# Kernel optimization log

Hardware: AMD Instinct MI355X
Metric: run time of the kernel (lower is better)

The kernel has to match this reference:

```python
import jax, jax.numpy as jnp
import numpy as np

XYZ_MIN = -1.0
XYZ_MAX = 1.0
ALPHA_INIT = 0.01
ACT_SHIFT = float(np.log(1.0 / (1.0 - ALPHA_INIT) - 1.0))  # density bias shift
INTERVAL = 0.5  # stepsize * voxel_size_ratio
VIEWBASE_PE = 4


def trilinear(grid, pts):
    """grid: [C,X,Y,Z]; pts: [...,3] in world coords; align_corners=True trilinear."""
    gs = grid.shape[1:]
    size_f = jnp.asarray(gs, pts.dtype)
    u = (pts - XYZ_MIN) / (XYZ_MAX - XYZ_MIN) * (size_f - 1.0)
    u = jnp.clip(u, 0.0, size_f - 1.0)
    i0 = jnp.floor(u).astype(jnp.int32)
    i0 = jnp.minimum(i0, jnp.asarray(gs, jnp.int32) - 2)
    f = u - i0.astype(pts.dtype)
    x0, y0, z0 = i0[..., 0], i0[..., 1], i0[..., 2]
    x1, y1, z1 = x0 + 1, y0 + 1, z0 + 1
    fx, fy, fz = f[..., 0, None], f[..., 1, None], f[..., 2, None]
    g = lambda ix, iy, iz: jnp.moveaxis(grid[:, ix, iy, iz], 0, -1)  # [...,C]
    c00 = g(x0, y0, z0) * (1 - fz) + g(x0, y0, z1) * fz
    c01 = g(x0, y1, z0) * (1 - fz) + g(x0, y1, z1) * fz
    c10 = g(x1, y0, z0) * (1 - fz) + g(x1, y0, z1) * fz
    c11 = g(x1, y1, z0) * (1 - fz) + g(x1, y1, z1) * fz
    c0 = c00 * (1 - fy) + c01 * fy
    c1 = c10 * (1 - fy) + c11 * fy
    return c0 * (1 - fx) + c1 * fx


def setup_inputs() -> dict:
    key = jax.random.key(0)
    ks = jax.random.split(key, 8)
    N, S, G, C, W = 4096, 256, 160, 12, 128
    dim0 = 3 + 3 * VIEWBASE_PE * 2 + C  # 39
    pts = jax.random.uniform(ks[0], (N, S, 3), jnp.float32, minval=-1.0, maxval=1.0)
    viewdirs = jax.random.normal(ks[1], (N, 3), jnp.float32)
    density_grid = jax.random.normal(ks[2], (1, G, G, G), jnp.float32)
    k0_grid = jax.random.normal(ks[3], (C, G, G, G), jnp.float32)
    w0 = jax.random.normal(ks[4], (dim0, W), jnp.float32) * 0.1
    w1 = jax.random.normal(ks[5], (W, W), jnp.float32) * 0.1
    w2 = jax.random.normal(ks[6], (W, 3), jnp.float32) * 0.1
    return dict(pts=pts, viewdirs=viewdirs, density_grid=density_grid, k0_grid=k0_grid,
                w0=w0, b0=jnp.zeros((W,), jnp.float32), w1=w1, b1=jnp.zeros((W,), jnp.float32),
                w2=w2, b2=jnp.zeros((3,), jnp.float32))


def reference(pts, viewdirs, density_grid, k0_grid, w0, b0, w1, b1, w2, b2):
    # --- density query + Raw2Alpha: alpha = 1 - (1+exp(d+shift))^(-interval) ---
    dens = trilinear(density_grid, pts)[..., 0]  # [N,S]
    alpha = 1.0 - jnp.exp(-jax.nn.softplus(dens + ACT_SHIFT) * INTERVAL)
    # --- Alphas2Weights: per-ray exclusive transmittance cumprod ---
    T = jnp.cumprod(1.0 - alpha, axis=1)  # [N,S]
    T_excl = jnp.concatenate([jnp.ones_like(T[:, :1]), T[:, :-1]], axis=1)
    weights = alpha * T_excl  # [N,S]
    alphainv_last = T[:, -1]  # [N]
    # --- color feature grid + view positional encoding ---
    k0 = trilinear(k0_grid, pts)  # [N,S,C]
    vd = viewdirs / jnp.linalg.norm(viewdirs, axis=-1, keepdims=True)  # [N,3]
    freqs = (2.0 ** jnp.arange(VIEWBASE_PE)).astype(vd.dtype)
    vf = (vd[..., None] * freqs).reshape(vd.shape[0], -1)  # [N,12]
    emb = jnp.concatenate([vd, jnp.sin(vf), jnp.cos(vf)], axis=-1)  # [N,27]
    feat = jnp.concatenate(
        [k0, jnp.broadcast_to(emb[:, None, :], k0.shape[:2] + (emb.shape[-1],))], axis=-1)  # [N,S,39]
    # --- rgbnet MLP (depth 3) ---
    h = jax.nn.relu(feat @ w0 + b0)
    h = jax.nn.relu(h @ w1 + b1)
    rgb = jax.nn.sigmoid(h @ w2 + b2)  # [N,S,3]
    # --- composite with white background ---
    rgb_marched = jnp.einsum('ns,nsc->nc', weights, rgb) + alphainv_last[:, None]
    return rgb_marched
```

## Files before the change

### kernel.cpp

```cpp
#include <hip/hip_runtime.h>

#define G      160
#define G3     (G*G*G)
#define NRAYS  4096
#define SAMP   256
#define CK0    12
#define HID    128

#define ACT_SHIFT (-4.59511985013459f)

#define FS 72
#define HS 136

typedef __attribute__((ext_vector_type(8))) short bf16x8;
typedef __attribute__((ext_vector_type(4))) float f32x4;

__device__ __forceinline__ unsigned short f2bf(float x) {
    unsigned u = __float_as_uint(x);
    unsigned r = u + 0x7fffu + ((u >> 16) & 1u);
    return (unsigned short)(r >> 16);
}
__device__ __forceinline__ float bflo(unsigned u) { return __uint_as_float(u << 16); }
__device__ __forceinline__ float bfhi(unsigned u) { return __uint_as_float(u & 0xffff0000u); }
__device__ __forceinline__ unsigned pack2(float a, float b) {
    return (unsigned)f2bf(a) | ((unsigned)f2bf(b) << 16);
}

__global__ __launch_bounds__(256) void prepass_kernel(
        const float* __restrict__ dgrid,
        const float* __restrict__ kgrid,
        unsigned short* __restrict__ vox)
{
    int v4 = (blockIdx.x * 256 + threadIdx.x) * 4;
    if (v4 >= G3) return;
    union F4 { float4 v; float f[4]; };
    F4 d; d.v = *reinterpret_cast<const float4*>(dgrid + v4);
    F4 kk[CK0];
#pragma unroll
    for (int c = 0; c < CK0; c++)
        kk[c].v = *reinterpret_cast<const float4*>(kgrid + (size_t)c * G3 + v4);
#pragma unroll
    for (int i = 0; i < 4; i++) {
        uint4 qa, qb;
        qa.x = pack2(d.f[i],      kk[0].f[i]);
        qa.y = pack2(kk[1].f[i],  kk[2].f[i]);
        qa.z = pack2(kk[3].f[i],  kk[4].f[i]);
        qa.w = pack2(kk[5].f[i],  kk[6].f[i]);
        qb.x = pack2(kk[7].f[i],  kk[8].f[i]);
        qb.y = pack2(kk[9].f[i],  kk[10].f[i]);
        qb.z = pack2(kk[11].f[i], 0.0f);
        qb.w = 0u;
        uint4* dst = reinterpret_cast<uint4*>(vox + (size_t)(v4 + i) * 16);
        dst[0] = qa;
        dst[1] = qb;
    }
}

__global__ void pack_weights(const float* __restrict__ w0,
                             const float* __restrict__ w1,
                             const float* __restrict__ w2,
                             unsigned short* __restrict__ w0p,
                             unsigned short* __restrict__ w1p,
                             unsigned short* __restrict__ w2p)
{
    int t = threadIdx.x;
    for (int idx = t; idx < 16 * 512; idx += 256) {
        int f = idx >> 9, r = idx & 511, l = r >> 3, j = r & 7;
        int nt = f >> 1, ks = f & 1;
        int k = ks * 32 + ((l >> 4) << 3) + j;
        int n = nt * 16 + (l & 15);
        w0p[idx] = (k < 39) ? f2bf(w0[k * HID + n]) : (unsigned short)0;
    }
    for (int idx = t; idx < 32 * 512; idx += 256) {
        int f = idx >> 9, r = idx & 511, l = r >> 3, j = r & 7;
        int nt = f >> 2, ks = f & 3;
        int k = ks * 32 + ((l >> 4) << 3) + j;
        int n = nt * 16 + (l & 15);
        w1p[idx] = f2bf(w1[k * HID + n]);
    }
    for (int idx = t; idx < 4 * 512; idx += 256) {
        int f = idx >> 9, r = idx & 511, l = r >> 3, j = r & 7;
        int ks = f;
        int k = ks * 32 + ((l >> 4) << 3) + j;
        int n = (l & 15);
        w2p[idx] = (n < 3) ? f2bf(w2[k * 3 + n]) : (unsigned short)0;
    }
}

__global__ __launch_bounds__(256) void dvgo_mfma(
        const float* __restrict__ pts,
        const float* __restrict__ viewdirs,
        const unsigned short* __restrict__ vox,
        const unsigned short* __restrict__ w0p,
        const unsigned short* __restrict__ w1p,
        const unsigned short* __restrict__ w2p,
        const float* __restrict__ b0, const float* __restrict__ b1,
        const float* __restrict__ b2,
        float* __restrict__ out)
{
    __shared__ unsigned short s_mem[SAMP * HS];
    __shared__ float s_alpha[SAMP];
    __shared__ float s_P[SAMP];
    __shared__ float s_out[4];

    const int n = blockIdx.x;
    const int t = threadIdx.x;
    const int lane = t & 63;
    const int wv = t >> 6;
    const int wbase = wv << 6;
    const int c    = lane & 15;
    const int quad = lane >> 4;

    if (t < 4) s_out[t] = 0.0f;

    const float* p = pts + ((size_t)n * SAMP + t) * 3;
    float pc[3] = {p[0], p[1], p[2]};
    int   i0[3];
    float fr[3];
#pragma unroll
    for (int d = 0; d < 3; d++) {
        float uu = (pc[d] + 1.0f) * 0.5f * (float)(G - 1);
        uu = fminf(fmaxf(uu, 0.0f), (float)(G - 1));
        int i = (int)floorf(uu);
        if (i > G - 2) i = G - 2;
        i0[d] = i;
        fr[d] = uu - (float)i;
    }

    float dens = 0.0f;
    float k0v[CK0];
#pragma unroll
    for (int ch = 0; ch < CK0; ch++) k0v[ch] = 0.0f;

#pragma unroll
    for (int cx = 0; cx < 2; cx++) {
        float wx = cx ? fr[0] : 1.0f - fr[0];
#pragma unroll
        for (int cy = 0; cy < 2; cy++) {
            float wxy = wx * (cy ? fr[1] : 1.0f - fr[1]);
#pragma unroll
            for (int cz = 0; cz < 2; cz++) {
                float wgt = wxy * (cz ? fr[2] : 1.0f - fr[2]);
                int vidx = ((i0[0] + cx) * G + (i0[1] + cy)) * G + (i0[2] + cz);
                const uint4* q = reinterpret_cast<const uint4*>(vox) + (size_t)vidx * 2;
                uint4 A = q[0];
                uint4 B = q[1];
                dens    += wgt * bflo(A.x);
                k0v[0]  += wgt * bfhi(A.x);
                k0v[1]  += wgt * bflo(A.y);
                k0v[2]  += wgt * bfhi(A.y);
                k0v[3]  += wgt * bflo(A.z);
                k0v[4]  += wgt * bfhi(A.z);
                k0v[5]  += wgt * bflo(A.w);
                k0v[6]  += wgt * bfhi(A.w);
                k0v[7]  += wgt * bflo(B.x);
                k0v[8]  += wgt * bfhi(B.x);
                k0v[9]  += wgt * bflo(B.y);
                k0v[10] += wgt * bfhi(B.y);
                k0v[11] += wgt * bflo(B.z);
            }
        }
    }

    float xs = dens + ACT_SHIFT;
    float sp = (xs > 20.0f) ? xs : log1pf(expf(xs));
    float alpha = 1.0f - expf(-sp * 0.5f);
    s_alpha[t] = alpha;
    s_P[t] = 1.0f - alpha;

    float v0 = viewdirs[n * 3 + 0];
    float v1 = viewdirs[n * 3 + 1];
    float v2 = viewdirs[n * 3 + 2];
    float inv = 1.0f / sqrtf(v0 * v0 + v1 * v1 + v2 * v2);
    v0 *= inv; v1 *= inv; v2 *= inv;

    float feat[40];
#pragma unroll
    for (int ch = 0; ch < CK0; ch++) feat[ch] = k0v[ch];
    feat[12] = v0; feat[13] = v1; feat[14] = v2;
    {
        float vd3[3] = {v0, v1, v2};
#pragma unroll
        for (int i = 0; i < 3; i++) {
#pragma unroll
            for (int j = 0; j < 4; j++) {
                float a = vd3[i] * (float)(1 << j);
                feat[15 + i * 4 + j] = sinf(a);
                feat[27 + i * 4 + j] = cosf(a);
            }
        }
    }
    feat[39] = 0.0f;

#pragma unroll
    for (int ch = 0; ch < 8; ch++) {
        uint4 q;
        if (ch < 5) {
            q.x = pack2(feat[ch * 8 + 0], feat[ch * 8 + 1]);
            q.y = pack2(feat[ch * 8 + 2], feat[ch * 8 + 3]);
            q.z = pack2(feat[ch * 8 + 4], feat[ch * 8 + 5]);
            q.w = pack2(feat[ch * 8 + 6], feat[ch * 8 + 7]);
        } else {
            q.x = 0u; q.y = 0u; q.z = 0u; q.w = 0u;
        }
        *reinterpret_cast<uint4*>(&s_mem[t * FS + ch * 8]) = q;
    }

    __syncthreads();
#pragma unroll
    for (int off = 1; off < SAMP; off <<= 1) {
        float v = (t >= off) ? s_P[t - off] : 1.0f;
        __syncthreads();
        s_P[t] *= v;
        __syncthreads();
    }

    const f32x4 zf = {0.0f, 0.0f, 0.0f, 0.0f};

    bf16x8 a1[4][2];
#pragma unroll
    for (int mt = 0; mt < 4; mt++)
#pragma unroll
        for (int ks = 0; ks < 2; ks++)
            a1[mt][ks] = *reinterpret_cast<const bf16x8*>(
                &s_mem[(wbase + mt * 16 + c) * FS + ks * 32 + quad * 8]);
    __syncthreads();

    const uint4* w0q = reinterpret_cast<const uint4*>(w0p);
#pragma unroll
    for (int nt = 0; nt < 8; nt++) {
        union { uint4 q; bf16x8 s; } bA, bB;
        bA.q = w0q[(nt * 2 + 0) * 64 + lane];
        bB.q = w0q[(nt * 2 + 1) * 64 + lane];
        f32x4 acc[4];
#pragma unroll
        for (int mt = 0; mt < 4; mt++) {
            f32x4 tmp = __builtin_amdgcn_mfma_f32_16x16x32_bf16(a1[mt][0], bA.s, zf, 0, 0, 0);
            acc[mt]   = __builtin_amdgcn_mfma_f32_16x16x32_bf16(a1[mt][1], bB.s, tmp, 0, 0, 0);
        }
        float bias = b0[nt * 16 + c];
#pragma unroll
        for (int mt = 0; mt < 4; mt++)
#pragma unroll
            for (int r = 0; r < 4; r++) {
                float h = fmaxf(acc[mt][r] + bias, 0.0f);
                s_mem[(wbase + mt * 16 + quad * 4 + r) * HS + nt * 16 + c] = f2bf(h);
            }
    }

    bf16x8 a2[4][4];
#pragma unroll
    for (int mt = 0; mt < 4; mt++)
#pragma unroll
        for (int ks = 0; ks < 4; ks++)
            a2[mt][ks] = *reinterpret_cast<const bf16x8*>(
                &s_mem[(wbase + mt * 16 + c) * HS + ks * 32 + quad * 8]);

    const uint4* w1q = reinterpret_cast<const uint4*>(w1p);
#pragma unroll
    for (int nt = 0; nt < 8; nt++) {
        f32x4 acc[4] = {zf, zf, zf, zf};
#pragma unroll
        for (int ks = 0; ks < 4; ks++) {
            union { uint4 q; bf16x8 s; } bb;
            bb.q = w1q[(nt * 4 + ks) * 64 + lane];
#pragma unroll
            for (int mt = 0; mt < 4; mt++)
                acc[mt] = __builtin_amdgcn_mfma_f32_16x16x32_bf16(a2[mt][ks], bb.s, acc[mt], 0, 0, 0);
        }
        float bias = b1[nt * 16 + c];
#pragma unroll
        for (int mt = 0; mt < 4; mt++)
#pragma unroll
            for (int r = 0; r < 4; r++) {
                float h = fmaxf(acc[mt][r] + bias, 0.0f);
                s_mem[(wbase + mt * 16 + quad * 4 + r) * HS + nt * 16 + c] = f2bf(h);
            }
    }

    bf16x8 a3[4][4];
#pragma unroll
    for (int mt = 0; mt < 4; mt++)
#pragma unroll
        for (int ks = 0; ks < 4; ks++)
            a3[mt][ks] = *reinterpret_cast<const bf16x8*>(
                &s_mem[(wbase + mt * 16 + c) * HS + ks * 32 + quad * 8]);

    const uint4* w2q = reinterpret_cast<const uint4*>(w2p);
    f32x4 acc3[4] = {zf, zf, zf, zf};
#pragma unroll
    for (int ks = 0; ks < 4; ks++) {
        union { uint4 q; bf16x8 s; } bb;
        bb.q = w2q[ks * 64 + lane];
#pragma unroll
        for (int mt = 0; mt < 4; mt++)
            acc3[mt] = __builtin_amdgcn_mfma_f32_16x16x32_bf16(a3[mt][ks], bb.s, acc3[mt], 0, 0, 0);
    }

    float b2c = (c < 3) ? b2[c] : 0.0f;
    float csum = 0.0f;
#pragma unroll
    for (int mt = 0; mt < 4; mt++)
#pragma unroll
        for (int r = 0; r < 4; r++) {
            int m = wbase + mt * 16 + quad * 4 + r;
            float pre = acc3[mt][r] + b2c;
            float sg = 1.0f / (1.0f + expf(-pre));
            float Texcl = (m == 0) ? 1.0f : s_P[m - 1];
            float wgt = s_alpha[m] * Texcl;
            csum += wgt * sg;
        }
    csum += __shfl_xor(csum, 16);
    csum += __shfl_xor(csum, 32);
    if (quad == 0 && c < 3) atomicAdd(&s_out[c], csum);
    __syncthreads();
    if (t < 3) out[n * 3 + t] = s_out[t] + s_P[SAMP - 1];
}

__global__ __launch_bounds__(256, 2) void dvgo_fallback(
        const float* __restrict__ pts, const float* __restrict__ viewdirs,
        const float* __restrict__ dgrid, const float* __restrict__ kgrid,
        const float* __restrict__ w0, const float* __restrict__ b0,
        const float* __restrict__ w1, const float* __restrict__ b1,
        const float* __restrict__ w2, const float* __restrict__ b2,
        float* __restrict__ out)
{
    const int n = blockIdx.x;
    const int t = threadIdx.x;
    __shared__ float  s_alpha[SAMP];
    __shared__ float  s_P[SAMP];
    __shared__ float  s_h1[SAMP * 33];
    __shared__ float  s_red[12];

    const float* p = pts + ((size_t)n * SAMP + t) * 3;
    float pc[3] = {p[0], p[1], p[2]};
    int i0[3]; float fr[3];
#pragma unroll
    for (int d = 0; d < 3; d++) {
        float uu = (pc[d] + 1.0f) * 0.5f * (float)(G - 1);
        uu = fminf(fmaxf(uu, 0.0f), (float)(G - 1));
        int i = (int)floorf(uu);
        if (i > G - 2) i = G - 2;
        i0[d] = i; fr[d] = uu - (float)i;
    }
    float dens = 0.0f, k0v[CK0];
#pragma unroll
    for (int ch = 0; ch < CK0; ch++) k0v[ch] = 0.0f;
#pragma unroll
    for (int cx = 0; cx < 2; cx++)
#pragma unroll
        for (int cy = 0; cy < 2; cy++)
#pragma unroll
            for (int cz = 0; cz < 2; cz++) {
                float w = (cx ? fr[0] : 1.0f - fr[0]) * (cy ? fr[1] : 1.0f - fr[1]) * (cz ? fr[2] : 1.0f - fr[2]);
                int vidx = ((i0[0] + cx) * G + (i0[1] + cy)) * G + (i0[2] + cz);
                dens += w * dgrid[vidx];
#pragma unroll
                for (int ch = 0; ch < CK0; ch++) k0v[ch] += w * kgrid[(size_t)ch * G3 + vidx];
            }
    float xs = dens + ACT_SHIFT;
    float sp = (xs > 20.0f) ? xs : log1pf(expf(xs));
    float alpha = 1.0f - expf(-sp * 0.5f);
    s_alpha[t] = alpha; s_P[t] = 1.0f - alpha;
    __syncthreads();
#pragma unroll
    for (int off = 1; off < SAMP; off <<= 1) {
        float v = (t >= off) ? s_P[t - off] : 1.0f;
        __syncthreads();
        s_P[t] *= v;
        __syncthreads();
    }
    float v0 = viewdirs[n * 3 + 0], v1 = viewdirs[n * 3 + 1], v2 = viewdirs[n * 3 + 2];
    float inv = 1.0f / sqrtf(v0 * v0 + v1 * v1 + v2 * v2);
    v0 *= inv; v1 *= inv; v2 *= inv;
    float feat[39];
#pragma unroll
    for (int ch = 0; ch < CK0; ch++) feat[ch] = k0v[ch];
    feat[12] = v0; feat[13] = v1; feat[14] = v2;
    float vd3[3] = {v0, v1, v2};
#pragma unroll
    for (int i = 0; i < 3; i++)
#pragma unroll
        for (int j = 0; j < 4; j++) {
            float a = vd3[i] * (float)(1 << j);
            feat[15 + i * 4 + j] = sinf(a);
            feat[27 + i * 4 + j] = cosf(a);
        }
    float h1[HID];
#pragma unroll 1
    for (int ch = 0; ch < 4; ch++) {
        float acc[32];
#pragma unroll
        for (int j = 0; j < 32; j++) acc[j] = b0[ch * 32 + j];
#pragma unroll
        for (int k = 0; k < 39; k++) {
            float f = feat[k];
#pragma unroll
            for (int j = 0; j < 32; j++) acc[j] = fmaf(f, w0[k * HID + ch * 32 + j], acc[j]);
        }
#pragma unroll
        for (int j = 0; j < 32; j++) h1[ch * 32 + j] = fmaxf(acc[j], 0.0f);
    }
    float rgbpre[3] = {b2[0], b2[1], b2[2]};
#pragma unroll 1
    for (int ch = 0; ch < 4; ch++) {
        float acc[32];
#pragma unroll
        for (int j = 0; j < 32; j++) acc[j] = b1[ch * 32 + j];
#pragma unroll 4
        for (int k = 0; k < HID; k++) {
            float hk = h1[k];
#pragma unroll
            for (int j = 0; j < 32; j++) acc[j] = fmaf(hk, w1[k * HID + ch * 32 + j], acc[j]);
        }
#pragma unroll
        for (int j = 0; j < 32; j++) {
            float h2 = fmaxf(acc[j], 0.0f);
            int jj = ch * 32 + j;
            rgbpre[0] = fmaf(h2, w2[jj * 3 + 0], rgbpre[0]);
            rgbpre[1] = fmaf(h2, w2[jj * 3 + 1], rgbpre[1]);
            rgbpre[2] = fmaf(h2, w2[jj * 3 + 2], rgbpre[2]);
        }
    }
    float T_excl = (t == 0) ? 1.0f : s_P[t - 1];
    float wgt = s_alpha[t] * T_excl;
    float c0 = wgt / (1.0f + expf(-rgbpre[0]));
    float c1 = wgt / (1.0f + expf(-rgbpre[1]));
    float c2 = wgt / (1.0f + expf(-rgbpre[2]));
#pragma unroll
    for (int off = 32; off > 0; off >>= 1) {
        c0 += __shfl_down(c0, off);
        c1 += __shfl_down(c1, off);
        c2 += __shfl_down(c2, off);
    }
    if ((t & 63) == 0) {
        int wv = t >> 6;
        s_red[wv * 3 + 0] = c0; s_red[wv * 3 + 1] = c1; s_red[wv * 3 + 2] = c2;
    }
    __syncthreads();
    if (t == 0) {
        float alast = s_P[SAMP - 1];
        float o0 = alast, o1 = alast, o2 = alast;
#pragma unroll
        for (int wv = 0; wv < 4; wv++) {
            o0 += s_red[wv * 3 + 0]; o1 += s_red[wv * 3 + 1]; o2 += s_red[wv * 3 + 2];
        }
        out[n * 3 + 0] = o0; out[n * 3 + 1] = o1; out[n * 3 + 2] = o2;
    }
    (void)s_h1;
}

extern "C" void kernel_launch(void* const* d_in, const int* in_sizes, int n_in,
                              void* d_out, int out_size, void* d_ws, size_t ws_size,
                              hipStream_t stream) {
    const float* pts      = (const float*)d_in[0];
    const float* viewdirs = (const float*)d_in[1];
    const float* dgrid    = (const float*)d_in[2];
    const float* kgrid    = (const float*)d_in[3];
    const float* w0       = (const float*)d_in[4];
    const float* b0       = (const float*)d_in[5];
    const float* w1       = (const float*)d_in[6];
    const float* b1       = (const float*)d_in[7];
    const float* w2       = (const float*)d_in[8];
    const float* b2       = (const float*)d_in[9];
    float* out = (float*)d_out;

    const size_t VOXB = (size_t)G3 * 32;
    const size_t W0PE = 16 * 512, W1PE = 32 * 512, W2PE = 4 * 512;
    const size_t TOTB = VOXB + (W0PE + W1PE + W2PE) * 2;

    if (ws_size >= TOTB) {
        unsigned short* vox  = (unsigned short*)d_ws;
        unsigned short* w0pp = (unsigned short*)((char*)d_ws + VOXB);
        unsigned short* w1pp = w0pp + W0PE;
        unsigned short* w2pp = w1pp + W1PE;
        prepass_kernel<<<G3 / 4 / 256, 256, 0, stream>>>(dgrid, kgrid, vox);
        pack_weights<<<1, 256, 0, stream>>>(w0, w1, w2, w0pp, w1pp, w2pp);
        dvgo_mfma<<<NRAYS, 256, 0, stream>>>(pts, viewdirs, vox, w0pp, w1pp, w2pp,
                                             b0, b1, b2, out);
    } else {
        dvgo_fallback<<<NRAYS, SAMP, 0, stream>>>(pts, viewdirs, dgrid, kgrid,
                                                  w0, b0, w1, b1, w2, b2, out);
    }
}
```

Baseline: 551.5 us.

## Switch to fp16 MFMA, wave-scan transmittance, per-wave LDS slabs, parallel weight packing

Replaces bf16 storage and MFMA with fp16 (pkrtz conversion, half2 FMA trilinear accumulation) and moves density into the last half of each voxel record. The shared-memory cumprod with many block barriers becomes a wave shuffle scan plus a cross-wave prefix, and precomputed weights are stored once. The view-direction embedding is computed by a few threads and broadcast, per-wave LDS slabs remove block-wide syncs, and weight packing now runs over many blocks. Fast intrinsics (__expf, __logf, __sinf) replace precise ones, and fp16 accumulation of features adds precision and range risk.

Result: faster. 519.7 us (-5.8%).

```diff
diff --git a/kernel.cpp b/kernel.cpp
--- a/kernel.cpp
+++ b/kernel.cpp
@@ -1,4 +1,5 @@
 #include <hip/hip_runtime.h>
+#include <hip/hip_fp16.h>
 
 #define G      160
 #define G3     (G*G*G)
@@ -11,19 +12,16 @@
 
 #define FS 72
 #define HS 136
-
-typedef __attribute__((ext_vector_type(8))) short bf16x8;
-typedef __attribute__((ext_vector_type(4))) float f32x4;
-
-__device__ __forceinline__ unsigned short f2bf(float x) {
-    unsigned u = __float_as_uint(x);
-    unsigned r = u + 0x7fffu + ((u >> 16) & 1u);
-    return (unsigned short)(r >> 16);
-}
-__device__ __forceinline__ float bflo(unsigned u) { return __uint_as_float(u << 16); }
-__device__ __forceinline__ float bfhi(unsigned u) { return __uint_as_float(u & 0xffff0000u); }
-__device__ __forceinline__ unsigned pack2(float a, float b) {
-    return (unsigned)f2bf(a) | ((unsigned)f2bf(b) << 16);
+#define SLABH (64 * HS)
+
+typedef __attribute__((ext_vector_type(8))) _Float16 f16x8;
+typedef __attribute__((ext_vector_type(4))) float    f32x4;
+
+__device__ __forceinline__ unsigned pkrtz_u(float a, float b) {
+    typedef __attribute__((ext_vector_type(2))) __fp16 fp16v2;
+    union { fp16v2 h; unsigned u; } cv;
+    cv.h = __builtin_amdgcn_cvt_pkrtz(a, b);
+    return cv.u;
 }
 
 __global__ __launch_bounds__(256) void prepass_kernel(
@@ -42,48 +40,51 @@
 #pragma unroll
     for (int i = 0; i < 4; i++) {
         uint4 qa, qb;
-        qa.x = pack2(d.f[i],      kk[0].f[i]);
-        qa.y = pack2(kk[1].f[i],  kk[2].f[i]);
-        qa.z = pack2(kk[3].f[i],  kk[4].f[i]);
-        qa.w = pack2(kk[5].f[i],  kk[6].f[i]);
-        qb.x = pack2(kk[7].f[i],  kk[8].f[i]);
-        qb.y = pack2(kk[9].f[i],  kk[10].f[i]);
-        qb.z = pack2(kk[11].f[i], 0.0f);
-        qb.w = 0u;
+        qa.x = pkrtz_u(kk[0].f[i],  kk[1].f[i]);
+        qa.y = pkrtz_u(kk[2].f[i],  kk[3].f[i]);
+        qa.z = pkrtz_u(kk[4].f[i],  kk[5].f[i]);
+        qa.w = pkrtz_u(kk[6].f[i],  kk[7].f[i]);
+        qb.x = pkrtz_u(kk[8].f[i],  kk[9].f[i]);
+        qb.y = pkrtz_u(kk[10].f[i], kk[11].f[i]);
+        qb.z = 0u;
+        qb.w = pkrtz_u(0.0f, d.f[i]);
         uint4* dst = reinterpret_cast<uint4*>(vox + (size_t)(v4 + i) * 16);
         dst[0] = qa;
         dst[1] = qb;
     }
 }
 
-__global__ void pack_weights(const float* __restrict__ w0,
-                             const float* __restrict__ w1,
-                             const float* __restrict__ w2,
-                             unsigned short* __restrict__ w0p,
-                             unsigned short* __restrict__ w1p,
-                             unsigned short* __restrict__ w2p)
+#define W0PE (16 * 512)
+#define W1PE (32 * 512)
+#define W2PE (4 * 512)
+__global__ __launch_bounds__(256) void pack_weights(
+        const float* __restrict__ w0, const float* __restrict__ w1,
+        const float* __restrict__ w2,
+        unsigned short* __restrict__ w0p, unsigned short* __restrict__ w1p,
+        unsigned short* __restrict__ w2p)
 {
-    int t = threadIdx.x;
-    for (int idx = t; idx < 16 * 512; idx += 256) {
+    int idx = blockIdx.x * 256 + threadIdx.x;
+    if (idx < W0PE) {
         int f = idx >> 9, r = idx & 511, l = r >> 3, j = r & 7;
         int nt = f >> 1, ks = f & 1;
         int k = ks * 32 + ((l >> 4) << 3) + j;
-        int n = nt * 16 + (l & 15);
-        w0p[idx] = (k < 39) ? f2bf(w0[k * HID + n]) : (unsigned short)0;
-    }
-    for (int idx = t; idx < 32 * 512; idx += 256) {
-        int f = idx >> 9, r = idx & 511, l = r >> 3, j = r & 7;
+        int nn = nt * 16 + (l & 15);
+        w0p[idx] = (k < 39) ? __half_as_ushort(__float2half(w0[k * HID + nn]))
+                            : (unsigned short)0;
+    } else if (idx < W0PE + W1PE) {
+        int m = idx - W0PE;
+        int f = m >> 9, r = m & 511, l = r >> 3, j = r & 7;
         int nt = f >> 2, ks = f & 3;
         int k = ks * 32 + ((l >> 4) << 3) + j;
-        int n = nt * 16 + (l & 15);
-        w1p[idx] = f2bf(w1[k * HID + n]);
-    }
-    for (int idx = t; idx < 4 * 512; idx += 256) {
-        int f = idx >> 9, r = idx & 511, l = r >> 3, j = r & 7;
-        int ks = f;
+        int nn = nt * 16 + (l & 15);
+        w1p[m] = __half_as_ushort(__float2half(w1[k * HID + nn]));
+    } else if (idx < W0PE + W1PE + W2PE) {
+        int m = idx - W0PE - W1PE;
+        int ks = m >> 9, r = m & 511, l = r >> 3, j = r & 7;
         int k = ks * 32 + ((l >> 4) << 3) + j;
-        int n = (l & 15);
-        w2p[idx] = (n < 3) ? f2bf(w2[k * 3 + n]) : (unsigned short)0;
+        int nn = l & 15;
+        w2p[m] = (nn < 3) ? __half_as_ushort(__float2half(w2[k * 3 + nn]))
+                          : (unsigned short)0;
     }
 }
 
@@ -98,20 +99,43 @@
         const float* __restrict__ b2,
         float* __restrict__ out)
 {
-    __shared__ unsigned short s_mem[SAMP * HS];
-    __shared__ float s_alpha[SAMP];
-    __shared__ float s_P[SAMP];
-    __shared__ float s_out[4];
-
-    const int n = blockIdx.x;
-    const int t = threadIdx.x;
+    __shared__ __half s_mem[4 * SLABH];
+    __shared__ float  s_wgt[SAMP];
+    __shared__ float  s_wave[4];
+    __shared__ unsigned s_u[16];
+    __shared__ float  s_out[4];
+
+    const int n    = blockIdx.x;
+    const int t    = threadIdx.x;
     const int lane = t & 63;
-    const int wv = t >> 6;
+    const int wv   = t >> 6;
     const int wbase = wv << 6;
     const int c    = lane & 15;
     const int quad = lane >> 4;
+    __half* slab = s_mem + wv * SLABH;
+    const int lr = lane;
 
     if (t < 4) s_out[t] = 0.0f;
+
+    if (t < 14) {
+        float v0 = viewdirs[n * 3 + 0];
+        float v1 = viewdirs[n * 3 + 1];
+        float v2 = viewdirs[n * 3 + 2];
+        float inv = rsqrtf(v0 * v0 + v1 * v1 + v2 * v2);
+        float vd[3] = {v0 * inv, v1 * inv, v2 * inv};
+        float fv[2];
+#pragma unroll
+        for (int e = 0; e < 2; e++) {
+            int col = 12 + 2 * t + e;
+            float f;
+            if (col < 15)      f = vd[col - 12];
+            else if (col < 27) { int s = col - 15; f = __sinf(vd[s >> 2] * (float)(1 << (s & 3))); }
+            else if (col < 39) { int s = col - 27; f = __cosf(vd[s >> 2] * (float)(1 << (s & 3))); }
+            else               f = 0.0f;
+            fv[e] = f;
+        }
+        s_u[t + 2] = pkrtz_u(fv[0], fv[1]);
+    }
 
     const float* p = pts + ((size_t)n * SAMP + t) * 3;
     float pc[3] = {p[0], p[1], p[2]};
@@ -127,10 +151,9 @@
         fr[d] = uu - (float)i;
     }
 
+    __half2 accA0 = __float2half2_rn(0.0f), accA1 = accA0, accA2 = accA0, accA3 = accA0;
+    __half2 accB0 = accA0, accB1 = accA0;
     float dens = 0.0f;
-    float k0v[CK0];
-#pragma unroll
-    for (int ch = 0; ch < CK0; ch++) k0v[ch] = 0.0f;
 
 #pragma unroll
     for (int cx = 0; cx < 2; cx++) {
@@ -140,121 +163,105 @@
             float wxy = wx * (cy ? fr[1] : 1.0f - fr[1]);
 #pragma unroll
             for (int cz = 0; cz < 2; cz++) {
-                float wgt = wxy * (cz ? fr[2] : 1.0f - fr[2]);
+                float w = wxy * (cz ? fr[2] : 1.0f - fr[2]);
                 int vidx = ((i0[0] + cx) * G + (i0[1] + cy)) * G + (i0[2] + cz);
                 const uint4* q = reinterpret_cast<const uint4*>(vox) + (size_t)vidx * 2;
-                uint4 A = q[0];
-                uint4 B = q[1];
-                dens    += wgt * bflo(A.x);
-                k0v[0]  += wgt * bfhi(A.x);
-                k0v[1]  += wgt * bflo(A.y);
-                k0v[2]  += wgt * bfhi(A.y);
-                k0v[3]  += wgt * bflo(A.z);
-                k0v[4]  += wgt * bfhi(A.z);
-                k0v[5]  += wgt * bflo(A.w);
-                k0v[6]  += wgt * bfhi(A.w);
-                k0v[7]  += wgt * bflo(B.x);
-                k0v[8]  += wgt * bfhi(B.x);
-                k0v[9]  += wgt * bflo(B.y);
-                k0v[10] += wgt * bfhi(B.y);
-                k0v[11] += wgt * bflo(B.z);
+                union { uint4 q; __half2 h2[4]; } A, B;
+                A.q = q[0];
+                B.q = q[1];
+                __half2 wh = __half2half2(__float2half(w));
+                accA0 = __hfma2(wh, A.h2[0], accA0);
+                accA1 = __hfma2(wh, A.h2[1], accA1);
+                accA2 = __hfma2(wh, A.h2[2], accA2);
+                accA3 = __hfma2(wh, A.h2[3], accA3);
+                accB0 = __hfma2(wh, B.h2[0], accB0);
+                accB1 = __hfma2(wh, B.h2[1], accB1);
+                dens += w * __half2float(__high2half(B.h2[3]));
             }
         }
     }
 
     float xs = dens + ACT_SHIFT;
-    float sp = (xs > 20.0f) ? xs : log1pf(expf(xs));
-    float alpha = 1.0f - expf(-sp * 0.5f);
-    s_alpha[t] = alpha;
-    s_P[t] = 1.0f - alpha;
-
-    float v0 = viewdirs[n * 3 + 0];
-    float v1 = viewdirs[n * 3 + 1];
-    float v2 = viewdirs[n * 3 + 2];
-    float inv = 1.0f / sqrtf(v0 * v0 + v1 * v1 + v2 * v2);
-    v0 *= inv; v1 *= inv; v2 *= inv;
-
-    float feat[40];
-#pragma unroll
-    for (int ch = 0; ch < CK0; ch++) feat[ch] = k0v[ch];
-    feat[12] = v0; feat[13] = v1; feat[14] = v2;
+    float sp = fmaxf(xs, 0.0f) + __logf(1.0f + __expf(-fabsf(xs)));
+    float alpha = 1.0f - __expf(-sp * 0.5f);
+
+    float xi = 1.0f - alpha;
+#pragma unroll
+    for (int off = 1; off < 64; off <<= 1) {
+        float y = __shfl_up(xi, off);
+        if (lane >= off) xi *= y;
+    }
+    if (lane == 63) s_wave[wv] = xi;
+
+    __syncthreads();
+
+    float prefix = 1.0f;
+#pragma unroll
+    for (int u = 0; u < 3; u++)
+        if (u < wv) prefix *= s_wave[u];
+    float xp = __shfl_up(xi, 1);
+    float Texcl = prefix * ((lane == 0) ? 1.0f : xp);
+    s_wgt[t] = alpha * Texcl;
+
     {
-        float vd3[3] = {v0, v1, v2};
-#pragma unroll
-        for (int i = 0; i < 3; i++) {
-#pragma unroll
-            for (int j = 0; j < 4; j++) {
-                float a = vd3[i] * (float)(1 << j);
-                feat[15 + i * 4 + j] = sinf(a);
-                feat[27 + i * 4 + j] = cosf(a);
-            }
-        }
-    }
-    feat[39] = 0.0f;
-
-#pragma unroll
-    for (int ch = 0; ch < 8; ch++) {
-        uint4 q;
-        if (ch < 5) {
-            q.x = pack2(feat[ch * 8 + 0], feat[ch * 8 + 1]);
-            q.y = pack2(feat[ch * 8 + 2], feat[ch * 8 + 3]);
-            q.z = pack2(feat[ch * 8 + 4], feat[ch * 8 + 5]);
-            q.w = pack2(feat[ch * 8 + 6], feat[ch * 8 + 7]);
-        } else {
-            q.x = 0u; q.y = 0u; q.z = 0u; q.w = 0u;
-        }
-        *reinterpret_cast<uint4*>(&s_mem[t * FS + ch * 8]) = q;
-    }
-
-    __syncthreads();
-#pragma unroll
-    for (int off = 1; off < SAMP; off <<= 1) {
-        float v = (t >= off) ? s_P[t - off] : 1.0f;
-        __syncthreads();
-        s_P[t] *= v;
-        __syncthreads();
+        uint4 q0, q1;
+        union { __half2 h; unsigned u; } cv;
+        cv.h = accA0; q0.x = cv.u;
+        cv.h = accA1; q0.y = cv.u;
+        cv.h = accA2; q0.z = cv.u;
+        cv.h = accA3; q0.w = cv.u;
+        cv.h = accB0; q1.x = cv.u;
+        cv.h = accB1; q1.y = cv.u;
+        q1.z = s_u[2];
+        q1.w = s_u[3];
+        *reinterpret_cast<uint4*>(slab + lr * FS)     = q0;
+        *reinterpret_cast<uint4*>(slab + lr * FS + 8) = q1;
+        const uint4* uq = reinterpret_cast<const uint4*>(s_u);
+        *reinterpret_cast<uint4*>(slab + lr * FS + 16) = uq[1];
+        *reinterpret_cast<uint4*>(slab + lr * FS + 24) = uq[2];
+        *reinterpret_cast<uint4*>(slab + lr * FS + 32) = uq[3];
     }
 
     const f32x4 zf = {0.0f, 0.0f, 0.0f, 0.0f};
-
-    bf16x8 a1[4][2];
-#pragma unroll
-    for (int mt = 0; mt < 4; mt++)
-#pragma unroll
-        for (int ks = 0; ks < 2; ks++)
-            a1[mt][ks] = *reinterpret_cast<const bf16x8*>(
-                &s_mem[(wbase + mt * 16 + c) * FS + ks * 32 + quad * 8]);
-    __syncthreads();
+    const f16x8 zfrag = {};
+
+    f16x8 a1[4][2];
+#pragma unroll
+    for (int mt = 0; mt < 4; mt++) {
+        a1[mt][0] = *reinterpret_cast<const f16x8*>(slab + (mt * 16 + c) * FS + quad * 8);
+        a1[mt][1] = zfrag;
+        if (quad == 0)
+            a1[mt][1] = *reinterpret_cast<const f16x8*>(slab + (mt * 16 + c) * FS + 32);
+    }
 
     const uint4* w0q = reinterpret_cast<const uint4*>(w0p);
 #pragma unroll
     for (int nt = 0; nt < 8; nt++) {
-        union { uint4 q; bf16x8 s; } bA, bB;
+        union { uint4 q; f16x8 s; } bA, bB;
         bA.q = w0q[(nt * 2 + 0) * 64 + lane];
         bB.q = w0q[(nt * 2 + 1) * 64 + lane];
         f32x4 acc[4];
 #pragma unroll
         for (int mt = 0; mt < 4; mt++) {
-            f32x4 tmp = __builtin_amdgcn_mfma_f32_16x16x32_bf16(a1[mt][0], bA.s, zf, 0, 0, 0);
-            acc[mt]   = __builtin_amdgcn_mfma_f32_16x16x32_bf16(a1[mt][1], bB.s, tmp, 0, 0, 0);
+            f32x4 tmp = __builtin_amdgcn_mfma_f32_16x16x32_f16(a1[mt][0], bA.s, zf, 0, 0, 0);
+            acc[mt]   = __builtin_amdgcn_mfma_f32_16x16x32_f16(a1[mt][1], bB.s, tmp, 0, 0, 0);
         }
         float bias = b0[nt * 16 + c];
 #pragma unroll
         for (int mt = 0; mt < 4; mt++)
 #pragma unroll
-            for (int r = 0; r < 4; r++) {
-                float h = fmaxf(acc[mt][r] + bias, 0.0f);
-                s_mem[(wbase + mt * 16 + quad * 4 + r) * HS + nt * 16 + c] = f2bf(h);
-            }
-    }
-
-    bf16x8 a2[4][4];
+            for (int r = 0; r < 4; r++)
+                slab[(mt * 16 + quad * 4 + r) * HS + nt * 16 + c] =
+                    __float2half(fmaxf(acc[mt][r] + bias, 0.0f));
+    }
+
+    f16x8 a2[4][4];
 #pragma unroll
     for (int mt = 0; mt < 4; mt++)
 #pragma unroll
         for (int ks = 0; ks < 4; ks++)
-            a2[mt][ks] = *reinterpret_cast<const bf16x8*>(
-                &s_mem[(wbase + mt * 16 + c) * HS + ks * 32 + quad * 8]);
+            a2[mt][ks] = *reinterpret_cast<const f16x8*>(
+                slab + (mt * 16 + c) * HS + ks * 32 + quad * 8);
 
     const uint4* w1q = reinterpret_cast<const uint4*>(w1p);
 #pragma unroll
@@ -262,39 +269,38 @@
         f32x4 acc[4] = {zf, zf, zf, zf};
 #pragma unroll
         for (int ks = 0; ks < 4; ks++) {
-            union { uint4 q; bf16x8 s; } bb;
+            union { uint4 q; f16x8 s; } bb;
             bb.q = w1q[(nt * 4 + ks) * 64 + lane];
 #pragma unroll
             for (int mt = 0; mt < 4; mt++)
-                acc[mt] = __builtin_amdgcn_mfma_f32_16x16x32_bf16(a2[mt][ks], bb.s, acc[mt], 0, 0, 0);
+                acc[mt] = __builtin_amdgcn_mfma_f32_16x16x32_f16(a2[mt][ks], bb.s, acc[mt], 0, 0, 0);
         }
         float bias = b1[nt * 16 + c];
 #pragma unroll
         for (int mt = 0; mt < 4; mt++)
 #pragma unroll
-            for (int r = 0; r < 4; r++) {
-                float h = fmaxf(acc[mt][r] + bias, 0.0f);
-                s_mem[(wbase + mt * 16 + quad * 4 + r) * HS + nt * 16 + c] = f2bf(h);
-            }
-    }
-
-    bf16x8 a3[4][4];
+            for (int r = 0; r < 4; r++)
+                slab[(mt * 16 + quad * 4 + r) * HS + nt * 16 + c] =
+                    __float2half(fmaxf(acc[mt][r] + bias, 0.0f));
+    }
+
+    f16x8 a3[4][4];
 #pragma unroll
     for (int mt = 0; mt < 4; mt++)
 #pragma unroll
         for (int ks = 0; ks < 4; ks++)
-            a3[mt][ks] = *reinterpret_cast<const bf16x8*>(
-                &s_mem[(wbase + mt * 16 + c) * HS + ks * 32 + quad * 8]);
+            a3[mt][ks] = *reinterpret_cast<const f16x8*>(
+                slab + (mt * 16 + c) * HS + ks * 32 + quad * 8);
 
     const uint4* w2q = reinterpret_cast<const uint4*>(w2p);
     f32x4 acc3[4] = {zf, zf, zf, zf};
 #pragma unroll
     for (int ks = 0; ks < 4; ks++) {
-        union { uint4 q; bf16x8 s; } bb;
+        union { uint4 q; f16x8 s; } bb;
         bb.q = w2q[ks * 64 + lane];
 #pragma unroll
         for (int mt = 0; mt < 4; mt++)
-            acc3[mt] = __builtin_amdgcn_mfma_f32_16x16x32_bf16(a3[mt][ks], bb.s, acc3[mt], 0, 0, 0);
+            acc3[mt] = __builtin_amdgcn_mfma_f32_16x16x32_f16(a3[mt][ks], bb.s, acc3[mt], 0, 0, 0);
     }
 
     float b2c = (c < 3) ? b2[c] : 0.0f;
@@ -305,16 +311,18 @@
         for (int r = 0; r < 4; r++) {
             int m = wbase + mt * 16 + quad * 4 + r;
             float pre = acc3[mt][r] + b2c;
-            float sg = 1.0f / (1.0f + expf(-pre));
-            float Texcl = (m == 0) ? 1.0f : s_P[m - 1];
-            float wgt = s_alpha[m] * Texcl;
-            csum += wgt * sg;
+            float sg = 1.0f / (1.0f + __expf(-pre));
+            csum += s_wgt[m] * sg;
         }
     csum += __shfl_xor(csum, 16);
     csum += __shfl_xor(csum, 32);
     if (quad == 0 && c < 3) atomicAdd(&s_out[c], csum);
+
     __syncthreads();
-    if (t < 3) out[n * 3 + t] = s_out[t] + s_P[SAMP - 1];
+    if (t < 3) {
+        float alast = s_wave[0] * s_wave[1] * s_wave[2] * s_wave[3];
+        out[n * 3 + t] = s_out[t] + alast;
+    }
 }
 
 __global__ __launch_bounds__(256, 2) void dvgo_fallback(
@@ -327,10 +335,9 @@
 {
     const int n = blockIdx.x;
     const int t = threadIdx.x;
-    __shared__ float  s_alpha[SAMP];
-    __shared__ float  s_P[SAMP];
-    __shared__ float  s_h1[SAMP * 33];
-    __shared__ float  s_red[12];
+    __shared__ float s_alpha[SAMP];
+    __shared__ float s_P[SAMP];
+    __shared__ float s_red[12];
 
     const float* p = pts + ((size_t)n * SAMP + t) * 3;
     float pc[3] = {p[0], p[1], p[2]};
@@ -434,20 +441,19 @@
         c2 += __shfl_down(c2, off);
     }
     if ((t & 63) == 0) {
-        int wv = t >> 6;
-        s_red[wv * 3 + 0] = c0; s_red[wv * 3 + 1] = c1; s_red[wv * 3 + 2] = c2;
+        int wvv = t >> 6;
+        s_red[wvv * 3 + 0] = c0; s_red[wvv * 3 + 1] = c1; s_red[wvv * 3 + 2] = c2;
     }
     __syncthreads();
     if (t == 0) {
         float alast = s_P[SAMP - 1];
         float o0 = alast, o1 = alast, o2 = alast;
 #pragma unroll
-        for (int wv = 0; wv < 4; wv++) {
-            o0 += s_red[wv * 3 + 0]; o1 += s_red[wv * 3 + 1]; o2 += s_red[wv * 3 + 2];
+        for (int wvv = 0; wvv < 4; wvv++) {
+            o0 += s_red[wvv * 3 + 0]; o1 += s_red[wvv * 3 + 1]; o2 += s_red[wvv * 3 + 2];
         }
         out[n * 3 + 0] = o0; out[n * 3 + 1] = o1; out[n * 3 + 2] = o2;
     }
-    (void)s_h1;
 }
 
 extern "C" void kernel_launch(void* const* d_in, const int* in_sizes, int n_in,
@@ -466,8 +472,7 @@
     float* out = (float*)d_out;
 
     const size_t VOXB = (size_t)G3 * 32;
-    const size_t W0PE = 16 * 512, W1PE = 32 * 512, W2PE = 4 * 512;
-    const size_t TOTB = VOXB + (W0PE + W1PE + W2PE) * 2;
+    const size_t TOTB = VOXB + (size_t)(W0PE + W1PE + W2PE) * 2;
 
     if (ws_size >= TOTB) {
         unsigned short* vox  = (unsigned short*)d_ws;
@@ -475,7 +480,8 @@
         unsigned short* w1pp = w0pp + W0PE;
         unsigned short* w2pp = w1pp + W1PE;
         prepass_kernel<<<G3 / 4 / 256, 256, 0, stream>>>(dgrid, kgrid, vox);
-        pack_weights<<<1, 256, 0, stream>>>(w0, w1, w2, w0pp, w1pp, w2pp);
+        pack_weights<<<(W0PE + W1PE + W2PE + 255) / 256, 256, 0, stream>>>(
+            w0, w1, w2, w0pp, w1pp, w2pp);
         dvgo_mfma<<<NRAYS, 256, 0, stream>>>(pts, viewdirs, vox, w0pp, w1pp, w2pp,
                                              b0, b1, b2, out);
     } else {
```
